# Kernel tuning notes

Hardware: AMD Instinct MI355X
Metric: run time of the kernel (lower is better)

Reference implementation:

```python
import jax, jax.numpy as jnp
import numpy as np

N = 100000   # total nodes across all graphs
E = 200000   # directed edges
B = 128      # number of graphs in the batch
IN1, IN2 = 128, 128
IN = IN1 + IN2      # in_feats = 256 (x || x_da)
HID = 64
OUT = 64


def setup_inputs() -> dict:
    key = jax.random.key(0)
    ks = jax.random.split(key, 6)
    x = jax.random.normal(ks[0], (N, IN1), jnp.float32)
    x_da = jax.random.normal(ks[1], (N, IN2), jnp.float32)
    edge_index = jax.random.randint(ks[2], (2, E), 0, N, dtype=jnp.int32)
    # equal, sorted, non-empty segments (graph ids) -- mirrors sorted PyG batch vector
    batch = (jnp.arange(N, dtype=jnp.int32) * B) // N
    # root node of graph b = first node of its segment
    rootindex = (jnp.arange(B, dtype=jnp.int32) * N) // B
    s1 = 1.0 / np.sqrt(IN)
    W1 = jax.random.uniform(ks[3], (IN, HID), jnp.float32, -s1, s1)
    b1 = jnp.zeros((HID,), jnp.float32)
    s2 = 1.0 / np.sqrt(HID + IN)
    W2 = jax.random.uniform(ks[4], (HID + IN, OUT), jnp.float32, -s2, s2)
    b2 = jnp.zeros((OUT,), jnp.float32)
    return dict(x=x, x_da=x_da, edge_index=edge_index, batch=batch,
                rootindex=rootindex, W1=W1, b1=b1, W2=W2, b2=b2)


def gcn_conv(x, edge_index, W, b):
    """PyG GCNConv: symmetric-normalized A+I message passing after a linear."""
    n = x.shape[0]
    h = x @ W                                   # [n, out] linear first (as in PyG)
    src, dst = edge_index[0], edge_index[1]
    # degree on target nodes, +1 for the added self loop
    deg = jnp.zeros((n,), h.dtype).at[dst].add(jnp.ones((src.shape[0],), h.dtype)) + 1.0
    dinv = jax.lax.rsqrt(deg)
    norm = dinv[src] * dinv[dst]                # [E]
    agg = jnp.zeros_like(h).at[dst].add(h[src] * norm[:, None])
    agg = agg + h * (dinv * dinv)[:, None]      # self-loop term: 1/deg
    return agg + b


def reference(x, x_da, edge_index, batch, rootindex, W1, b1, W2, b2):
    x0 = jnp.concatenate([x, x_da], axis=1)     # [N, IN]
    x1 = x0                                     # saved original features
    h = gcn_conv(x0, edge_index, W1, b1)        # [N, HID]
    x2 = h                                      # saved conv1 output
    # vectorized root-feature broadcast: replaces the python per-graph loop
    root1 = x1[rootindex[batch]]                # [N, IN]
    h = jax.nn.relu(jnp.concatenate([h, root1], axis=1))  # [N, HID+IN]
    # F.dropout with training=False is identity (eval mode)
    h = gcn_conv(h, edge_index, W2, b2)         # [N, OUT]
    h = jax.nn.relu(h)
    root2 = x2[rootindex[batch]]                # [N, HID]
    h = jnp.concatenate([h, root2], axis=1)     # [N, OUT+HID]
    # scatter_mean over graph ids
    sums = jax.ops.segment_sum(h, batch, num_segments=B)
    counts = jax.ops.segment_sum(jnp.ones((h.shape[0], 1), h.dtype), batch, num_segments=B)
    return sums / counts                        # [B, OUT+HID]
```

## Files before the change

### kernel.cpp

```cpp
#include <hip/hip_runtime.h>

#define IN1 128
#define K1 256
#define HID 64

typedef __attribute__((ext_vector_type(8))) __bf16 bf16x8;
typedef __attribute__((ext_vector_type(4))) __bf16 bf16x4;
typedef __attribute__((ext_vector_type(4))) float f32x4;

__device__ __forceinline__ int swz(int row, int k, int ldk) {
    return (row * ldk + k) ^ ((row & 7) << 3);
}

__global__ __launch_bounds__(256) void count_edges(const int* __restrict__ ei, int* counts, int E) {
    int e = blockIdx.x * 256 + threadIdx.x;
    if (e < E) atomicAdd(&counts[ei[E + e]], 1);
}

__global__ __launch_bounds__(256) void block_sums_dinv(const int* __restrict__ counts,
                                                       int* __restrict__ bsum,
                                                       float* __restrict__ dinv, int N) {
    __shared__ int sh[256];
    int i = blockIdx.x * 256 + threadIdx.x;
    int v = (i < N) ? counts[i] : 0;
    if (i < N) dinv[i] = rsqrtf((float)v + 1.0f);
    sh[threadIdx.x] = v;
    __syncthreads();
    for (int off = 128; off > 0; off >>= 1) {
        if (threadIdx.x < off) sh[threadIdx.x] += sh[threadIdx.x + off];
        __syncthreads();
    }
    if (threadIdx.x == 0) bsum[blockIdx.x] = sh[0];
}

__global__ __launch_bounds__(512) void scan_and_segs(const int* __restrict__ bsum,
                                                     int* __restrict__ boff, int nb,
                                                     const int* __restrict__ batch,
                                                     int* __restrict__ segs, int N, int B) {
    if (blockIdx.x == 0) {
        __shared__ int sh[512];
        int t = threadIdx.x;
        int v = (t < nb) ? bsum[t] : 0;
        sh[t] = v;
        __syncthreads();
        for (int off = 1; off < 512; off <<= 1) {
            int u = (t >= off) ? sh[t - off] : 0;
            __syncthreads();
            sh[t] += u;
            __syncthreads();
        }
        if (t < nb) boff[t] = sh[t] - v;
    } else {
        int b = threadIdx.x;
        if (b > B) return;
        if (b == B) { segs[B] = N; return; }
        int lo = 0, hi = N;
        while (lo < hi) {
            int mid = (lo + hi) >> 1;
            if (batch[mid] < b) lo = mid + 1; else hi = mid;
        }
        segs[b] = lo;
    }
}

__global__ __launch_bounds__(256) void write_rowstart(const int* __restrict__ counts,
                                                      const int* __restrict__ boff,
                                                      int* __restrict__ rowstart, int N, int E) {
    __shared__ int sh[256];
    int i = blockIdx.x * 256 + threadIdx.x;
    int t = threadIdx.x;
    int v = (i < N) ? counts[i] : 0;
    sh[t] = v;
    __syncthreads();
    for (int off = 1; off < 256; off <<= 1) {
        int u = (t >= off) ? sh[t - off] : 0;
        __syncthreads();
        sh[t] += u;
        __syncthreads();
    }
    if (i < N) rowstart[i] = boff[blockIdx.x] + sh[t] - v;
    if (i == 0) rowstart[N] = E;
}

__global__ __launch_bounds__(256) void scatter_csr(const int* __restrict__ ei,
                                                   const int* __restrict__ rowstart,
                                                   const float* __restrict__ dinv,
                                                   int* counts,
                                                   int* __restrict__ csr_src,
                                                   float* __restrict__ csr_w, int E) {
    int e = blockIdx.x * 256 + threadIdx.x;
    if (e >= E) return;
    int s = ei[e], d = ei[E + e];
    int pos = rowstart[d] + atomicSub(&counts[d], 1) - 1;
    csr_src[pos] = s;
    csr_w[pos] = dinv[s];
}

__global__ __launch_bounds__(256) void prep_fused(const float* __restrict__ W1,
                                                  const float* __restrict__ W2,
                                                  __bf16* __restrict__ w1img,
                                                  __bf16* __restrict__ w2img,
                                                  const float* __restrict__ x,
                                                  const float* __restrict__ xda,
                                                  const int* __restrict__ rootindex,
                                                  float* __restrict__ rb2) {
    int blk = blockIdx.x;
    if (blk < 80) {
        int tid = blk * 256 + threadIdx.x;
        if (tid < 64 * K1) {
            int k = tid >> 6, n = tid & 63;
            w1img[swz(n, k, K1)] = (__bf16)W1[tid];
        } else if (tid < 64 * K1 + 64 * 64) {
            int e = tid - 64 * K1;
            int k = e >> 6, n = e & 63;
            w2img[swz(n, k, 64)] = (__bf16)W2[e];
        }
    } else {
        int b = blk - 80;
        int root = rootindex[b];
        int j = threadIdx.x & 63, q = threadIdx.x >> 6;
        const float* xr = x + (size_t)root * IN1;
        const float* dr = xda + (size_t)root * IN1;
        float acc = 0.f;
        for (int kk = 0; kk < 64; ++kk) {
            int k = q * 64 + kk;
            float v = (k < IN1) ? xr[k] : dr[k - IN1];
            v = fmaxf(v, 0.f);
            acc = fmaf(v, W2[(size_t)(HID + k) * HID + j], acc);
        }
        __shared__ float sh[4][64];
        sh[q][j] = acc;
        __syncthreads();
        if (q == 0) rb2[b * HID + j] = sh[0][j] + sh[1][j] + sh[2][j] + sh[3][j];
    }
}

__global__ __launch_bounds__(256, 4) void gemm1_mfma(const float* __restrict__ x,
                                                     const float* __restrict__ xda,
                                                     const __bf16* __restrict__ w1img,
                                                     __bf16* __restrict__ h1, int N) {
    __shared__ __bf16 Ws[64 * K1];
    int tid = threadIdx.x;
#pragma unroll
    for (int i = 0; i < 8; ++i)
        reinterpret_cast<bf16x8*>(Ws)[i * 256 + tid] =
            reinterpret_cast<const bf16x8*>(w1img)[i * 256 + tid];
    __syncthreads();

    int w = tid >> 6, l = tid & 63;
    int lr = l & 15, lg = l >> 4;
    int arow = blockIdx.x * 64 + w * 16 + lr;
    int carow = min(arow, N - 1);
    const float4* px = reinterpret_cast<const float4*>(x + (size_t)carow * IN1) + lg * 2;
    const float4* pd = reinterpret_cast<const float4*>(xda + (size_t)carow * IN1) + lg * 2;

    f32x4 acc[4] = {};
    float4 buf[4][2];

#pragma unroll
    for (int t = 0; t < 4; ++t) {
        const float4* p = px + t * 8;
        buf[t][0] = p[0];
        buf[t][1] = p[1];
    }
#pragma unroll
    for (int t = 0; t < 8; ++t) {
        float4 fa = buf[t & 3][0], fb = buf[t & 3][1];
        if (t + 4 < 8) {
            int tn = t + 4;
            const float4* p = pd + (tn - 4) * 8;
            buf[t & 3][0] = p[0];
            buf[t & 3][1] = p[1];
        }
        bf16x8 af;
        af[0] = (__bf16)fa.x; af[1] = (__bf16)fa.y;
        af[2] = (__bf16)fa.z; af[3] = (__bf16)fa.w;
        af[4] = (__bf16)fb.x; af[5] = (__bf16)fb.y;
        af[6] = (__bf16)fb.z; af[7] = (__bf16)fb.w;
        int k0 = t * 32 + lg * 8;
#pragma unroll
        for (int c = 0; c < 4; ++c) {
            bf16x8 bfr = *reinterpret_cast<const bf16x8*>(&Ws[swz(c * 16 + lr, k0, K1)]);
            acc[c] = __builtin_amdgcn_mfma_f32_16x16x32_bf16(af, bfr, acc[c], 0, 0, 0);
        }
    }
#pragma unroll
    for (int c = 0; c < 4; ++c)
#pragma unroll
        for (int r = 0; r < 4; ++r) {
            int row = blockIdx.x * 64 + w * 16 + lg * 4 + r;
            if (row < N) h1[(size_t)row * HID + c * 16 + lr] = (__bf16)acc[c][r];
        }
}

__global__ __launch_bounds__(1024, 4) void conv2_fused(const int* __restrict__ rowstart,
                                                       const int* __restrict__ csr_src,
                                                       const float* __restrict__ csr_w,
                                                       const __bf16* __restrict__ h1,
                                                       const float* __restrict__ dinv,
                                                       const float* __restrict__ bias1,
                                                       const __bf16* __restrict__ w2img,
                                                       const float* __restrict__ rb2,
                                                       const int* __restrict__ batch,
                                                       const int* __restrict__ rootindex,
                                                       __bf16* __restrict__ h2,
                                                       float* __restrict__ rootx2, int N, int B) {
    __shared__ __bf16 As[64 * 64];
    __shared__ __bf16 Ws[64 * 64];
    int tid = threadIdx.x;
    if (tid < 512)
        reinterpret_cast<bf16x8*>(Ws)[tid] = reinterpret_cast<const bf16x8*>(w2img)[tid];

    int nb0 = blockIdx.x * 64;
    int ln = tid >> 4, cq = tid & 15;
    int i = nb0 + ln;
    bool ok = i < N;
    int ci = ok ? i : N - 1;
    float di = dinv[ci];
    float s2 = di * di;
    bf16x4 hv = *reinterpret_cast<const bf16x4*>(h1 + (size_t)ci * HID + cq * 4);
    float4 bv = reinterpret_cast<const float4*>(bias1)[cq];
    float a0 = fmaf((float)hv[0], s2, bv.x);
    float a1 = fmaf((float)hv[1], s2, bv.y);
    float a2 = fmaf((float)hv[2], s2, bv.z);
    float a3 = fmaf((float)hv[3], s2, bv.w);
    int k0 = rowstart[ci], k1 = rowstart[ci + 1];
    for (int k = k0; k < k1; ++k) {
        int s = csr_src[k];
        float wgt = csr_w[k] * di;
        bf16x4 sv = *reinterpret_cast<const bf16x4*>(h1 + (size_t)s * HID + cq * 4);
        a0 = fmaf((float)sv[0], wgt, a0);
        a1 = fmaf((float)sv[1], wgt, a1);
        a2 = fmaf((float)sv[2], wgt, a2);
        a3 = fmaf((float)sv[3], wgt, a3);
    }
    if (ok) {
        int lo = 0, hi = B - 1, bfound = -1;
        while (lo <= hi) {
            int mid = (lo + hi) >> 1;
            int rv = rootindex[mid];
            if (rv == i) { bfound = mid; break; }
            if (rv < i) lo = mid + 1; else hi = mid - 1;
        }
        if (bfound >= 0) {
            float4 o = make_float4(a0, a1, a2, a3);
            reinterpret_cast<float4*>(rootx2 + (size_t)bfound * 64)[cq] = o;
        }
    }
    bf16x4 rl;
    rl[0] = (__bf16)fmaxf(a0, 0.f); rl[1] = (__bf16)fmaxf(a1, 0.f);
    rl[2] = (__bf16)fmaxf(a2, 0.f); rl[3] = (__bf16)fmaxf(a3, 0.f);
    *reinterpret_cast<bf16x4*>(&As[swz(ln, cq * 4, 64)]) = rl;
    __syncthreads();

    int w = tid >> 6;
    int rg = w >> 2, cb = w & 3;
    int l = tid & 63, lr = l & 15, lg = l >> 4;
    f32x4 acc = {};
#pragma unroll
    for (int t = 0; t < 2; ++t) {
        int kk = t * 32 + lg * 8;
        bf16x8 af = *reinterpret_cast<const bf16x8*>(&As[swz(rg * 16 + lr, kk, 64)]);
        bf16x8 bfr = *reinterpret_cast<const bf16x8*>(&Ws[swz(cb * 16 + lr, kk, 64)]);
        acc = __builtin_amdgcn_mfma_f32_16x16x32_bf16(af, bfr, acc, 0, 0, 0);
    }
#pragma unroll
    for (int r = 0; r < 4; ++r) {
        int row = nb0 + rg * 16 + lg * 4 + r;
        if (row >= N) continue;
        int b = batch[row];
        h2[(size_t)row * HID + cb * 16 + lr] =
            (__bf16)(acc[r] + rb2[(size_t)b * HID + cb * 16 + lr]);
    }
}

__global__ __launch_bounds__(1024, 4) void conv3_mean(const int* __restrict__ rowstart,
                                                      const int* __restrict__ csr_src,
                                                      const float* __restrict__ csr_w,
                                                      const __bf16* __restrict__ h2,
                                                      const float* __restrict__ dinv,
                                                      const float* __restrict__ bias2,
                                                      const int* __restrict__ batch,
                                                      float* __restrict__ part, int N) {
    __shared__ float red[64][64];
    int tid = threadIdx.x;
    int nb0 = blockIdx.x * 64;
    int ln = tid >> 4, cq = tid & 15;
    int i = nb0 + ln;
    bool ok = i < N;
    int ci = ok ? i : N - 1;
    float di = dinv[ci];
    float s2 = di * di;
    bf16x4 hv = *reinterpret_cast<const bf16x4*>(h2 + (size_t)ci * HID + cq * 4);
    float4 bv = reinterpret_cast<const float4*>(bias2)[cq];
    float a0 = fmaf((float)hv[0], s2, bv.x);
    float a1 = fmaf((float)hv[1], s2, bv.y);
    float a2 = fmaf((float)hv[2], s2, bv.z);
    float a3 = fmaf((float)hv[3], s2, bv.w);
    int k0 = rowstart[ci], k1 = rowstart[ci + 1];
    for (int k = k0; k < k1; ++k) {
        int s = csr_src[k];
        float wgt = csr_w[k] * di;
        bf16x4 sv = *reinterpret_cast<const bf16x4*>(h2 + (size_t)s * HID + cq * 4);
        a0 = fmaf((float)sv[0], wgt, a0);
        a1 = fmaf((float)sv[1], wgt, a1);
        a2 = fmaf((float)sv[2], wgt, a2);
        a3 = fmaf((float)sv[3], wgt, a3);
    }
    float v0 = fmaxf(a0, 0.f), v1 = fmaxf(a1, 0.f);
    float v2 = fmaxf(a2, 0.f), v3 = fmaxf(a3, 0.f);

    int gme = ok ? batch[i] : -1;
    int g0 = batch[nb0];
    int gLast = batch[min(nb0 + 63, N - 1)];
    int g = g0;
    while (true) {
        float m = (gme == g) ? 1.f : 0.f;
        int f = cq * 4;
        red[ln][f + 0] = v0 * m;
        red[ln][f + 1] = v1 * m;
        red[ln][f + 2] = v2 * m;
        red[ln][f + 3] = v3 * m;
        __syncthreads();
#pragma unroll
        for (int off = 32; off > 0; off >>= 1) {
            if (ln < off) {
                red[ln][f + 0] += red[ln + off][f + 0];
                red[ln][f + 1] += red[ln + off][f + 1];
                red[ln][f + 2] += red[ln + off][f + 2];
                red[ln][f + 3] += red[ln + off][f + 3];
            }
            __syncthreads();
        }
        if (ln == 0) {
            atomicAdd(&part[(size_t)g * 64 + f + 0], red[0][f + 0]);
            atomicAdd(&part[(size_t)g * 64 + f + 1], red[0][f + 1]);
            atomicAdd(&part[(size_t)g * 64 + f + 2], red[0][f + 2]);
            atomicAdd(&part[(size_t)g * 64 + f + 3], red[0][f + 3]);
        }
        if (g == gLast) break;
        g = gLast;
        __syncthreads();
    }
}

__global__ __launch_bounds__(128) void mean_fin(const float* __restrict__ part,
                                                const float* __restrict__ rootx2,
                                                const int* __restrict__ segs,
                                                float* __restrict__ out) {
    int b = blockIdx.x;
    int f = threadIdx.x;
    if (f < 64)
        out[b * 128 + f] = part[(size_t)b * 64 + f] / (float)(segs[b + 1] - segs[b]);
    else
        out[b * 128 + f] = rootx2[(size_t)b * 64 + (f - 64)];
}

extern "C" void kernel_launch(void* const* d_in, const int* in_sizes, int n_in,
                              void* d_out, int out_size, void* d_ws, size_t ws_size,
                              hipStream_t stream) {
    const float* x    = (const float*)d_in[0];
    const float* xda  = (const float*)d_in[1];
    const int*   ei   = (const int*)d_in[2];
    const int*   batch= (const int*)d_in[3];
    const int*   root = (const int*)d_in[4];
    const float* W1   = (const float*)d_in[5];
    const float* b1   = (const float*)d_in[6];
    const float* W2   = (const float*)d_in[7];
    const float* b2   = (const float*)d_in[8];
    float* out = (float*)d_out;

    int N = in_sizes[3];
    int E = in_sizes[2] / 2;
    int B = in_sizes[4];

    int gN  = (N + 255) / 256;
    int gE  = (E + 255) / 256;
    int gM  = (N + 63) / 64;
    int nb  = gN;

    auto align = [](size_t v) { return (v + 255) & ~(size_t)255; };
    char* w = (char*)d_ws;
    int*   counts = (int*)w;    w += align((size_t)N * 4);
    float* part   = (float*)w;  w += align((size_t)B * 64 * 4);
    size_t zspan  = (char*)w - (char*)counts;
    float* dinv   = (float*)w;  w += align((size_t)N * 4);
    int*   rowst  = (int*)w;    w += align((size_t)(N + 1) * 4);
    int*   bsum   = (int*)w;    w += align((size_t)nb * 4);
    int*   boff   = (int*)w;    w += align((size_t)nb * 4);
    int*   csr_src= (int*)w;    w += align((size_t)E * 4);
    float* csr_w  = (float*)w;  w += align((size_t)E * 4);
    __bf16* bufA  = (__bf16*)w; w += align((size_t)N * HID * 2);
    __bf16* bufC  = (__bf16*)w; w += align((size_t)N * HID * 2);
    float* rootx2 = (float*)w;  w += align((size_t)B * 64 * 4);
    float* rb2    = (float*)w;  w += align((size_t)B * HID * 4);
    int*   segs   = (int*)w;    w += align((size_t)(B + 1) * 4);
    __bf16* w1img = (__bf16*)w; w += align((size_t)64 * K1 * 2);
    __bf16* w2img = (__bf16*)w; w += align((size_t)64 * 64 * 2);

    hipMemsetAsync(counts, 0, zspan, stream);
    count_edges<<<gE, 256, 0, stream>>>(ei, counts, E);
    block_sums_dinv<<<gN, 256, 0, stream>>>(counts, bsum, dinv, N);
    scan_and_segs<<<2, 512, 0, stream>>>(bsum, boff, nb, batch, segs, N, B);
    write_rowstart<<<gN, 256, 0, stream>>>(counts, boff, rowst, N, E);
    scatter_csr<<<gE, 256, 0, stream>>>(ei, rowst, dinv, counts, csr_src, csr_w, E);
    prep_fused<<<80 + B, 256, 0, stream>>>(W1, W2, w1img, w2img, x, xda, root, rb2);

    gemm1_mfma<<<gM, 256, 0, stream>>>(x, xda, w1img, bufA, N);

    conv2_fused<<<gM, 1024, 0, stream>>>(rowst, csr_src, csr_w, bufA, dinv, b1,
                                         w2img, rb2, batch, root, bufC, rootx2, N, B);

    conv3_mean<<<gM, 1024, 0, stream>>>(rowst, csr_src, csr_w, bufC, dinv, b2,
                                        batch, part, N);

    mean_fin<<<B, 128, 0, stream>>>(part, rootx2, segs, out);
}
```

Baseline: 235.9 us.

## Pack CSR src/weight into int2 and shrink aggregation blocks to 16 nodes

Merges the separate CSR source-index and weight arrays into a single interleaved int2 array, so each edge needs one 8-byte load instead of two scattered 4-byte loads. The conv2 and conv3 aggregation kernels also drop from 1024-thread blocks covering 64 nodes to 256-thread blocks covering 16 nodes. The smaller blocks are meant to cut barrier cost and let more blocks stay resident to hide gather latency. In exchange, each block reloads W2 into shared memory more often and issues more atomics to the per-graph partial sums.

```diff
diff --git a/kernel.cpp b/kernel.cpp
--- a/kernel.cpp
+++ b/kernel.cpp
@@ -86,14 +86,12 @@
                                                    const int* __restrict__ rowstart,
                                                    const float* __restrict__ dinv,
                                                    int* counts,
-                                                   int* __restrict__ csr_src,
-                                                   float* __restrict__ csr_w, int E) {
+                                                   int2* __restrict__ csr, int E) {
     int e = blockIdx.x * 256 + threadIdx.x;
     if (e >= E) return;
     int s = ei[e], d = ei[E + e];
     int pos = rowstart[d] + atomicSub(&counts[d], 1) - 1;
-    csr_src[pos] = s;
-    csr_w[pos] = dinv[s];
+    csr[pos] = make_int2(s, __float_as_int(dinv[s]));
 }
 
 __global__ __launch_bounds__(256) void prep_fused(const float* __restrict__ W1,
@@ -193,25 +191,26 @@
         }
 }
 
-__global__ __launch_bounds__(1024, 4) void conv2_fused(const int* __restrict__ rowstart,
-                                                       const int* __restrict__ csr_src,
-                                                       const float* __restrict__ csr_w,
-                                                       const __bf16* __restrict__ h1,
-                                                       const float* __restrict__ dinv,
-                                                       const float* __restrict__ bias1,
-                                                       const __bf16* __restrict__ w2img,
-                                                       const float* __restrict__ rb2,
-                                                       const int* __restrict__ batch,
-                                                       const int* __restrict__ rootindex,
-                                                       __bf16* __restrict__ h2,
-                                                       float* __restrict__ rootx2, int N, int B) {
-    __shared__ __bf16 As[64 * 64];
+__global__ __launch_bounds__(256, 8) void conv2_fused(const int* __restrict__ rowstart,
+                                                      const int2* __restrict__ csr,
+                                                      const __bf16* __restrict__ h1,
+                                                      const float* __restrict__ dinv,
+                                                      const float* __restrict__ bias1,
+                                                      const __bf16* __restrict__ w2img,
+                                                      const float* __restrict__ rb2,
+                                                      const int* __restrict__ batch,
+                                                      const int* __restrict__ rootindex,
+                                                      __bf16* __restrict__ h2,
+                                                      float* __restrict__ rootx2, int N, int B) {
+    __shared__ __bf16 As[16 * 64];
     __shared__ __bf16 Ws[64 * 64];
     int tid = threadIdx.x;
-    if (tid < 512)
-        reinterpret_cast<bf16x8*>(Ws)[tid] = reinterpret_cast<const bf16x8*>(w2img)[tid];
-
-    int nb0 = blockIdx.x * 64;
+#pragma unroll
+    for (int i = 0; i < 2; ++i)
+        reinterpret_cast<bf16x8*>(Ws)[i * 256 + tid] =
+            reinterpret_cast<const bf16x8*>(w2img)[i * 256 + tid];
+
+    int nb0 = blockIdx.x * 16;
     int ln = tid >> 4, cq = tid & 15;
     int i = nb0 + ln;
     bool ok = i < N;
@@ -226,9 +225,9 @@
     float a3 = fmaf((float)hv[3], s2, bv.w);
     int k0 = rowstart[ci], k1 = rowstart[ci + 1];
     for (int k = k0; k < k1; ++k) {
-        int s = csr_src[k];
-        float wgt = csr_w[k] * di;
-        bf16x4 sv = *reinterpret_cast<const bf16x4*>(h1 + (size_t)s * HID + cq * 4);
+        int2 e = csr[k];
+        float wgt = __int_as_float(e.y) * di;
+        bf16x4 sv = *reinterpret_cast<const bf16x4*>(h1 + (size_t)e.x * HID + cq * 4);
         a0 = fmaf((float)sv[0], wgt, a0);
         a1 = fmaf((float)sv[1], wgt, a1);
         a2 = fmaf((float)sv[2], wgt, a2);
@@ -253,20 +252,19 @@
     *reinterpret_cast<bf16x4*>(&As[swz(ln, cq * 4, 64)]) = rl;
     __syncthreads();
 
-    int w = tid >> 6;
-    int rg = w >> 2, cb = w & 3;
+    int cb = tid >> 6;
     int l = tid & 63, lr = l & 15, lg = l >> 4;
     f32x4 acc = {};
 #pragma unroll
     for (int t = 0; t < 2; ++t) {
         int kk = t * 32 + lg * 8;
-        bf16x8 af = *reinterpret_cast<const bf16x8*>(&As[swz(rg * 16 + lr, kk, 64)]);
+        bf16x8 af = *reinterpret_cast<const bf16x8*>(&As[swz(lr, kk, 64)]);
         bf16x8 bfr = *reinterpret_cast<const bf16x8*>(&Ws[swz(cb * 16 + lr, kk, 64)]);
         acc = __builtin_amdgcn_mfma_f32_16x16x32_bf16(af, bfr, acc, 0, 0, 0);
     }
 #pragma unroll
     for (int r = 0; r < 4; ++r) {
-        int row = nb0 + rg * 16 + lg * 4 + r;
+        int row = nb0 + lg * 4 + r;
         if (row >= N) continue;
         int b = batch[row];
         h2[(size_t)row * HID + cb * 16 + lr] =
@@ -274,17 +272,16 @@
     }
 }
 
-__global__ __launch_bounds__(1024, 4) void conv3_mean(const int* __restrict__ rowstart,
-                                                      const int* __restrict__ csr_src,
-                                                      const float* __restrict__ csr_w,
-                                                      const __bf16* __restrict__ h2,
-                                                      const float* __restrict__ dinv,
-                                                      const float* __restrict__ bias2,
-                                                      const int* __restrict__ batch,
-                                                      float* __restrict__ part, int N) {
-    __shared__ float red[64][64];
+__global__ __launch_bounds__(256, 8) void conv3_mean(const int* __restrict__ rowstart,
+                                                     const int2* __restrict__ csr,
+                                                     const __bf16* __restrict__ h2,
+                                                     const float* __restrict__ dinv,
+                                                     const float* __restrict__ bias2,
+                                                     const int* __restrict__ batch,
+                                                     float* __restrict__ part, int N) {
+    __shared__ float red[16][64];
     int tid = threadIdx.x;
-    int nb0 = blockIdx.x * 64;
+    int nb0 = blockIdx.x * 16;
     int ln = tid >> 4, cq = tid & 15;
     int i = nb0 + ln;
     bool ok = i < N;
@@ -299,9 +296,9 @@
     float a3 = fmaf((float)hv[3], s2, bv.w);
     int k0 = rowstart[ci], k1 = rowstart[ci + 1];
     for (int k = k0; k < k1; ++k) {
-        int s = csr_src[k];
-        float wgt = csr_w[k] * di;
-        bf16x4 sv = *reinterpret_cast<const bf16x4*>(h2 + (size_t)s * HID + cq * 4);
+        int2 e = csr[k];
+        float wgt = __int_as_float(e.y) * di;
+        bf16x4 sv = *reinterpret_cast<const bf16x4*>(h2 + (size_t)e.x * HID + cq * 4);
         a0 = fmaf((float)sv[0], wgt, a0);
         a1 = fmaf((float)sv[1], wgt, a1);
         a2 = fmaf((float)sv[2], wgt, a2);
@@ -312,7 +309,7 @@
 
     int gme = ok ? batch[i] : -1;
     int g0 = batch[nb0];
-    int gLast = batch[min(nb0 + 63, N - 1)];
+    int gLast = batch[min(nb0 + 15, N - 1)];
     int g = g0;
     while (true) {
         float m = (gme == g) ? 1.f : 0.f;
@@ -323,7 +320,7 @@
         red[ln][f + 3] = v3 * m;
         __syncthreads();
 #pragma unroll
-        for (int off = 32; off > 0; off >>= 1) {
+        for (int off = 8; off > 0; off >>= 1) {
             if (ln < off) {
                 red[ln][f + 0] += red[ln + off][f + 0];
                 red[ln][f + 1] += red[ln + off][f + 1];
@@ -377,6 +374,7 @@
     int gN  = (N + 255) / 256;
     int gE  = (E + 255) / 256;
     int gM  = (N + 63) / 64;
+    int gC  = (N + 15) / 16;
     int nb  = gN;
 
     auto align = [](size_t v) { return (v + 255) & ~(size_t)255; };
@@ -388,8 +386,7 @@
     int*   rowst  = (int*)w;    w += align((size_t)(N + 1) * 4);
     int*   bsum   = (int*)w;    w += align((size_t)nb * 4);
     int*   boff   = (int*)w;    w += align((size_t)nb * 4);
-    int*   csr_src= (int*)w;    w += align((size_t)E * 4);
-    float* csr_w  = (float*)w;  w += align((size_t)E * 4);
+    int2*  csr    = (int2*)w;   w += align((size_t)E * 8);
     __bf16* bufA  = (__bf16*)w; w += align((size_t)N * HID * 2);
     __bf16* bufC  = (__bf16*)w; w += align((size_t)N * HID * 2);
     float* rootx2 = (float*)w;  w += align((size_t)B * 64 * 4);
@@ -403,16 +400,16 @@
     block_sums_dinv<<<gN, 256, 0, stream>>>(counts, bsum, dinv, N);
     scan_and_segs<<<2, 512, 0, stream>>>(bsum, boff, nb, batch, segs, N, B);
     write_rowstart<<<gN, 256, 0, stream>>>(counts, boff, rowst, N, E);
-    scatter_csr<<<gE, 256, 0, stream>>>(ei, rowst, dinv, counts, csr_src, csr_w, E);
+    scatter_csr<<<gE, 256, 0, stream>>>(ei, rowst, dinv, counts, csr, E);
     prep_fused<<<80 + B, 256, 0, stream>>>(W1, W2, w1img, w2img, x, xda, root, rb2);
 
     gemm1_mfma<<<gM, 256, 0, stream>>>(x, xda, w1img, bufA, N);
 
-    conv2_fused<<<gM, 1024, 0, stream>>>(rowst, csr_src, csr_w, bufA, dinv, b1,
-                                         w2img, rb2, batch, root, bufC, rootx2, N, B);
-
-    conv3_mean<<<gM, 1024, 0, stream>>>(rowst, csr_src, csr_w, bufC, dinv, b2,
-                                        batch, part, N);
+    conv2_fused<<<gC, 256, 0, stream>>>(rowst, csr, bufA, dinv, b1,
+                                        w2img, rb2, batch, root, bufC, rootx2, N, B);
+
+    conv3_mean<<<gC, 256, 0, stream>>>(rowst, csr, bufC, dinv, b2,
+                                       batch, part, N);
 
     mean_fin<<<B, 128, 0, stream>>>(part, rootx2, segs, out);
 }
```

After: 239.1 us. No clear change (+1.3%).
